# Kernel tuning notes

Measured on AMD Instinct MI355X. Metric: run time of the kernel, lower is better.

## Reference

```python
import jax, jax.numpy as jnp
import numpy as np


def _f_map(x):
    # alpha = ||x||; x normalized; append a constant-1 feature
    alpha = jnp.linalg.norm(x, axis=-1, keepdims=True)
    xn = x / jnp.maximum(alpha, 1e-12)
    ones = jnp.ones(x.shape[:-1] + (1,), x.dtype)
    return jnp.concatenate([(1.0 - 0.5 ** alpha) * xn, ones], axis=-1)


def _mh_lka(q, k, v):
    # kernelized linear attention: cumsum of k (x) v outer products along seq
    q = _f_map(q)  # (B, N, D+1)
    k = _f_map(k)
    kv = jnp.cumsum(jnp.einsum('bnd,bne->bnde', k, v), axis=1)  # (B,N,D+1,D)
    k_ = jnp.cumsum(k, axis=1)
    qk = jnp.einsum('bnd,bnd->bn', q, k_)[..., None]
    qkv = jnp.einsum('bnd,bnde->bne', q, kv)
    return qkv / qk


def _lstm(x, Wih, Whh, bih, bhh):
    # single-layer batch-first LSTM, torch gate order (i, f, g, o)
    B, H = x.shape[0], Whh.shape[1]
    bias = bih + bhh
    def step(carry, xt):
        h, c = carry
        g = xt @ Wih.T + h @ Whh.T + bias  # (B, 4H)
        i, f, gg, o = jnp.split(g, 4, axis=-1)
        c = jax.nn.sigmoid(f) * c + jax.nn.sigmoid(i) * jnp.tanh(gg)
        h = jax.nn.sigmoid(o) * jnp.tanh(c)
        return (h, c), h
    h0 = jnp.zeros((B, H), x.dtype)
    c0 = jnp.zeros((B, H), x.dtype)
    _, hs = jax.lax.scan(step, (h0, c0), x.transpose(1, 0, 2))
    return hs.transpose(1, 0, 2)


def setup_inputs() -> dict:
    in_sz, hid, n_h, out_sz = 512, 64, 8, 512
    B, N = 2, 2048
    key = jax.random.key(0)
    ks = jax.random.split(key, 10)
    s = 0.02
    f32 = jnp.float32
    return {
        'x': jax.random.normal(ks[0], (B, N, in_sz), f32),
        'Wq': jax.random.normal(ks[1], (in_sz, hid * n_h), f32) * s,
        'bq': jnp.zeros((hid * n_h,), f32),
        'Wk': jax.random.normal(ks[2], (in_sz, hid * n_h), f32) * s,
        'bk': jnp.zeros((hid * n_h,), f32),
        'Wv': jax.random.normal(ks[3], (in_sz, hid * n_h), f32) * s,
        'bv': jnp.zeros((hid * n_h,), f32),
        'Wih': jax.random.normal(ks[4], (4 * hid, hid), f32) * s,
        'Whh': jax.random.normal(ks[5], (4 * hid, hid), f32) * s,
        'bih': jnp.zeros((4 * hid,), f32),
        'bhh': jnp.zeros((4 * hid,), f32),
        'W1': jax.random.normal(ks[6], (hid * n_h, out_sz), f32) * s,
        'b1': jnp.zeros((out_sz,), f32),
        'W2': jax.random.normal(ks[7], (out_sz, out_sz), f32) * s,
        'b2': jnp.zeros((out_sz,), f32),
        'gamma': jnp.ones((out_sz,), f32),
        'beta': jnp.zeros((out_sz,), f32),
    }


def reference(x, Wq, bq, Wk, bk, Wv, bv, Wih, Whh, bih, bhh, W1, b1, W2, b2, gamma, beta):
    B, N, _ = x.shape
    H = Whh.shape[1]
    n_h = Wq.shape[1] // H
    def proj(W, b_):
        y = x @ W + b_                              # (B, N, n_h*H)
        return y.reshape(B, N, n_h, H).transpose(0, 2, 1, 3).reshape(B * n_h, N, H)
    q, k, v = proj(Wq, bq), proj(Wk, bk), proj(Wv, bv)
    o = _mh_lka(q, k, v)                            # (B*n_h, N, H)
    o = o + _lstm(o, Wih, Whh, bih, bhh)
    o = o.reshape(B, n_h, N, H).transpose(0, 2, 1, 3).reshape(B, N, n_h * H)
    o = jax.nn.gelu(o @ W1 + b1, approximate=False) @ W2 + b2
    mu = o.mean(-1, keepdims=True)
    var = o.var(-1, keepdims=True)
    return (o - mu) / jnp.sqrt(var + 1e-5) * gamma + beta
```

## Files before the change

### kernel.cpp

```cpp
#include <hip/hip_runtime.h>
#include <hip/hip_bf16.h>
#include <hip/hip_fp16.h>

using bf16 = __hip_bfloat16;
using ushort_t = unsigned short;
using uint32 = unsigned int;
typedef _Float16 f16x2 __attribute__((ext_vector_type(2)));
typedef short short8 __attribute__((ext_vector_type(8)));
typedef float floatx4 __attribute__((ext_vector_type(4)));

__device__ __forceinline__ float u2f(ushort_t u) {
  return __uint_as_float(((unsigned int)u) << 16);
}
__device__ __forceinline__ bool probe_f32(const void* graw) {
  return ((const ushort_t*)graw)[0] != 0x3F80;
}
__device__ __forceinline__ float scrub(float v) {
  return fminf(fmaxf(v, -1e4f), 1e4f);
}
__device__ __forceinline__ short f2b(float x) {
  uint32 u = __float_as_uint(x);
  return (short)((u + 0x7FFFu + ((u >> 16) & 1u)) >> 16);
}
__device__ __forceinline__ float frcp(float x) {
#if __has_builtin(__builtin_amdgcn_rcpf)
  return __builtin_amdgcn_rcpf(x);
#else
  return 1.f / x;
#endif
}
template<int CTRL>
__device__ __forceinline__ float qperm(float x) {
  return __int_as_float(__builtin_amdgcn_mov_dpp(__float_as_int(x), CTRL, 0xF, 0xF, false));
}
__device__ __forceinline__ float fdot2(uint32 a, uint32 b, float c) {
#if __has_builtin(__builtin_amdgcn_fdot2)
  return __builtin_amdgcn_fdot2(__builtin_bit_cast(f16x2, a),
                                __builtin_bit_cast(f16x2, b), c, false);
#else
  const f16x2 av = __builtin_bit_cast(f16x2, a);
  const f16x2 bv = __builtin_bit_cast(f16x2, b);
  return c + (float)av[0] * (float)bv[0] + (float)av[1] * (float)bv[1];
#endif
}

struct Ptrs { const void* p[16]; };
__constant__ const int kCvtTotal = 1347584;

__global__ __launch_bounds__(256) void cvt_k(Ptrs ps, float* __restrict__ dst) {
  const int sizes[16] = {262144,512,262144,512,262144,512,16384,16384,
                         256,256,262144,512,262144,512,512,512};
  int idx = blockIdx.x * 256 + threadIdx.x;
  if (idx >= kCvtTotal) return;
  const bool f32in = probe_f32(ps.p[14]);
  int seg = 0, off = idx;
  while (off >= sizes[seg]) { off -= sizes[seg]; seg++; }
  float v;
  if (f32in) v = ((const float*)ps.p[seg])[off];
  else       v = u2f(((const ushort_t*)ps.p[seg])[off]);
  dst[idx] = v;
}

template<int AMODE, int ACT>
__global__ __launch_bounds__(256) void gemm_mfma(
    const void* __restrict__ A, const float* __restrict__ B,
    const float* __restrict__ bias, const void* __restrict__ graw,
    float* __restrict__ C, int M, int N, int K)
{
  __shared__ __align__(16) short As2[64][36];
  __shared__ __align__(16) short Bs2[64][36];
  const int t = threadIdx.x;
  const int row0 = blockIdx.y * 64, col0 = blockIdx.x * 64;
  const int w = t >> 6, lane = t & 63;
  const int quad = lane >> 4, lr = lane & 15;
  bool f32in = true;
  if (AMODE == 1) f32in = probe_f32(graw);

  const int am = t >> 2, akq = t & 3;
  const int bn = t & 63, bkq = t >> 6;

  floatx4 acc[4] = {{0,0,0,0},{0,0,0,0},{0,0,0,0},{0,0,0,0}};

  for (int k0 = 0; k0 < K; k0 += 32) {
    {
      const size_t aoff = (size_t)(row0 + am) * K + (k0 + akq * 8);
      short8 ap;
      if (AMODE == 0 || f32in) {
        const float4 v0 = *reinterpret_cast<const float4*>((const float*)A + aoff);
        const float4 v1 = *reinterpret_cast<const float4*>((const float*)A + aoff + 4);
        ap[0]=f2b(v0.x); ap[1]=f2b(v0.y); ap[2]=f2b(v0.z); ap[3]=f2b(v0.w);
        ap[4]=f2b(v1.x); ap[5]=f2b(v1.y); ap[6]=f2b(v1.z); ap[7]=f2b(v1.w);
      } else {
        const ushort4 u0 = *reinterpret_cast<const ushort4*>((const ushort_t*)A + aoff);
        const ushort4 u1 = *reinterpret_cast<const ushort4*>((const ushort_t*)A + aoff + 4);
        ap[0]=(short)u0.x; ap[1]=(short)u0.y; ap[2]=(short)u0.z; ap[3]=(short)u0.w;
        ap[4]=(short)u1.x; ap[5]=(short)u1.y; ap[6]=(short)u1.z; ap[7]=(short)u1.w;
      }
      *reinterpret_cast<short8*>(&As2[am][akq * 8]) = ap;
    }
    {
      const float* bp = B + (size_t)(k0 + bkq * 8) * N + col0 + bn;
      short8 bpk;
      #pragma unroll
      for (int j = 0; j < 8; j++) bpk[j] = f2b(bp[(size_t)j * N]);
      *reinterpret_cast<short8*>(&Bs2[bn][bkq * 8]) = bpk;
    }
    __syncthreads();
    {
      const short8 af = *reinterpret_cast<const short8*>(&As2[w * 16 + lr][quad * 8]);
      #pragma unroll
      for (int ct = 0; ct < 4; ct++) {
        const short8 bf = *reinterpret_cast<const short8*>(&Bs2[ct * 16 + lr][quad * 8]);
        acc[ct] = __builtin_amdgcn_mfma_f32_16x16x32_bf16(af, bf, acc[ct], 0, 0, 0);
      }
    }
    __syncthreads();
  }
  #pragma unroll
  for (int ct = 0; ct < 4; ct++) {
    const int col = col0 + ct * 16 + lr;
    const float bb = bias[col];
    #pragma unroll
    for (int r = 0; r < 4; r++) {
      const int row = row0 + w * 16 + quad * 4 + r;
      float v = acc[ct][r] + bb;
      if (ACT == 1) v = 0.5f * v * (1.0f + erff(v * 0.70710678118654752f));
      C[(size_t)row * N + col] = scrub(v);
    }
  }
}

__global__ __launch_bounds__(256) void attn_pass1(
    const float* __restrict__ kb, const float* __restrict__ vb,
    float* __restrict__ S, float* __restrict__ kcS)
{
  const int c = blockIdx.x, bh = blockIdx.y;
  const int b = bh >> 3, hd = bh & 7;
  const int t = threadIdx.x;
  const int e = t & 63, p = t >> 6;

  __shared__ __align__(16) float kf_s[2][64];
  __shared__ __align__(16) float v_s[2][64];

  float Sl[16], kcl[16], S64 = 0.f;
  #pragma unroll
  for (int i = 0; i < 16; i++) { Sl[i] = 0.f; kcl[i] = 0.f; }

  for (int nn = 0; nn < 64; nn++) {
    const int n = c * 64 + nn;
    const int buf = nn & 1;
    if (t < 64) {
      const size_t base = ((size_t)(b * 2048 + n)) * 512 + hd * 64 + t;
      const float kr = kb[base];
      const float vr = vb[base];
      float s = kr * kr;
      #pragma unroll
      for (int off = 32; off > 0; off >>= 1) s += __shfl_xor(s, off);
      const float ak = sqrtf(s);
      kf_s[buf][t] = (1.0f - exp2f(-ak)) / fmaxf(ak, 1e-12f) * kr;
      v_s[buf][t] = vr;
    }
    __syncthreads();
    const float ve = v_s[buf][e];
    #pragma unroll
    for (int i = 0; i < 16; i++) {
      const float kfd = kf_s[buf][p * 16 + i];
      Sl[i]  += kfd * ve;
      kcl[i] += kfd;
    }
    if (p == 0) S64 += ve;
  }
  const size_t sbase = ((size_t)(bh * 32 + c)) * 4160;
  #pragma unroll
  for (int i = 0; i < 16; i++) S[sbase + (p * 16 + i) * 64 + e] = Sl[i];
  if (p == 0) S[sbase + 4096 + e] = S64;
  if (e == 0) {
    const size_t kbase = ((size_t)(bh * 32 + c)) * 64;
    #pragma unroll
    for (int i = 0; i < 16; i++) kcS[kbase + p * 16 + i] = kcl[i];
  }
}

__global__ __launch_bounds__(256) void attn_pass2(
    float* __restrict__ S, float* __restrict__ kcS)
{
  const int bh = blockIdx.y;
  const int idx = blockIdx.x * 256 + threadIdx.x;
  if (idx < 4160) {
    const size_t base = (size_t)bh * 32 * 4160 + idx;
    float v[32];
    #pragma unroll
    for (int cc = 0; cc < 32; cc++) v[cc] = S[base + (size_t)cc * 4160];
    float run = 0.f;
    #pragma unroll
    for (int cc = 0; cc < 32; cc++) { const float tmp = v[cc]; v[cc] = run; run += tmp; }
    #pragma unroll
    for (int cc = 0; cc < 32; cc++) S[base + (size_t)cc * 4160] = v[cc];
  }
  if (blockIdx.x == 0 && threadIdx.x < 64) {
    const size_t base = (size_t)bh * 32 * 64 + threadIdx.x;
    float v[32];
    #pragma unroll
    for (int cc = 0; cc < 32; cc++) v[cc] = kcS[base + (size_t)cc * 64];
    float run = 0.f;
    #pragma unroll
    for (int cc = 0; cc < 32; cc++) { const float tmp = v[cc]; v[cc] = run; run += tmp; }
    #pragma unroll
    for (int cc = 0; cc < 32; cc++) kcS[base + (size_t)cc * 64] = v[cc];
  }
}

__global__ __launch_bounds__(256) void attn_pass3(
    const float* __restrict__ qb, const float* __restrict__ kb, const float* __restrict__ vb,
    const float* __restrict__ S, const float* __restrict__ kcS,
    float* __restrict__ ao)
{
  const int c = blockIdx.x, bh = blockIdx.y;
  const int b = bh >> 3, hd = bh & 7;
  const int t = threadIdx.x;
  const int e = t & 63, p = t >> 6;

  __shared__ __align__(16) float kf_s[2][64], qf_s[2][64], v_s[2][64];
  __shared__ __align__(16) float accp_s[2][4][64];
  __shared__ float qkp_s[2][4];

  float Sl[16], kcl[16], S64;
  {
    const size_t sbase = ((size_t)(bh * 32 + c)) * 4160;
    #pragma unroll
    for (int i = 0; i < 16; i++) Sl[i] = S[sbase + (p * 16 + i) * 64 + e];
    S64 = S[sbase + 4096 + e];
    const size_t kbase = ((size_t)(bh * 32 + c)) * 64;
    #pragma unroll
    for (int i = 0; i < 16; i++) kcl[i] = kcS[kbase + p * 16 + i];
  }

  for (int nn = 0; nn < 64; nn++) {
    const int n = c * 64 + nn;
    const int buf = nn & 1;
    if (t < 64) {
      const size_t base = ((size_t)(b * 2048 + n)) * 512 + hd * 64 + t;
      const float qr = qb[base];
      const float kr = kb[base];
      const float vr = vb[base];
      float sq = qr * qr, sk = kr * kr;
      #pragma unroll
      for (int off = 32; off > 0; off >>= 1) {
        sq += __shfl_xor(sq, off);
        sk += __shfl_xor(sk, off);
      }
      const float aq = sqrtf(sq), ak = sqrtf(sk);
      qf_s[buf][t] = (1.0f - exp2f(-aq)) / fmaxf(aq, 1e-12f) * qr;
      kf_s[buf][t] = (1.0f - exp2f(-ak)) / fmaxf(ak, 1e-12f) * kr;
      v_s[buf][t] = vr;
    }
    __syncthreads();
    const float ve = v_s[buf][e];
    float accp = 0.f, qkp = 0.f;
    #pragma unroll
    for (int i = 0; i < 16; i++) {
      const float kfd = kf_s[buf][p * 16 + i];
      const float qfd = qf_s[buf][p * 16 + i];
      Sl[i]  += kfd * ve;
      accp   += qfd * Sl[i];
      kcl[i] += kfd;
      qkp    += qfd * kcl[i];
    }
    if (p == 0) {
      S64  += ve;
      accp += S64;
      qkp  += (float)(n + 1);
    }
    accp_s[buf][p][e] = accp;
    if (e == 0) qkp_s[buf][p] = qkp;
    __syncthreads();
    if (t < 64) {
      const float num = accp_s[buf][0][t] + accp_s[buf][1][t] +
                        accp_s[buf][2][t] + accp_s[buf][3][t];
      float den = qkp_s[buf][0] + qkp_s[buf][1] + qkp_s[buf][2] + qkp_s[buf][3];
      den = fmaxf(den, 1e-6f);
      ao[((size_t)(bh * 2048 + n)) * 64 + t] = scrub(num / den);
    }
  }
}

__global__ __launch_bounds__(256) void gatesin_k(
    const float* __restrict__ ao, const float* __restrict__ Wihf,
    const float* __restrict__ bihf, const float* __restrict__ bhhf,
    __half* __restrict__ G)
{
  const int t = threadIdx.x;
  const int row0 = blockIdx.x * 16;
  __shared__ __align__(16) float o_s[16 * 64];
  __shared__ __align__(16) __half g_s[16 * 256];
  {
    const float4 v = *reinterpret_cast<const float4*>(ao + (size_t)row0 * 64 + t * 4);
    *reinterpret_cast<float4*>(&o_s[t * 4]) = v;
  }
  float w[64];
  #pragma unroll
  for (int e = 0; e < 64; e++) w[e] = Wihf[t * 64 + e];
  const float bias = bihf[t] + bhhf[t];
  __syncthreads();
  const int p = (t & 63) * 4 + (t >> 6);
  for (int r = 0; r < 16; r++) {
    float acc = bias;
    #pragma unroll
    for (int e4 = 0; e4 < 16; e4++) {
      const float4 o4 = *reinterpret_cast<const float4*>(&o_s[r * 64 + e4 * 4]);
      acc += w[e4*4+0]*o4.x + w[e4*4+1]*o4.y + w[e4*4+2]*o4.z + w[e4*4+3]*o4.w;
    }
    g_s[r * 256 + p] = __float2half(acc);
  }
  __syncthreads();
  const uint4* src = reinterpret_cast<const uint4*>(&g_s[0]);
  uint4* dst = reinterpret_cast<uint4*>(G + (size_t)row0 * 256);
  dst[t] = src[t];
  dst[t + 256] = src[t + 256];
}

__global__ __attribute__((amdgpu_flat_work_group_size(256, 256), amdgpu_waves_per_eu(1, 1)))
void lstm_k(
    const float* __restrict__ ao, const __half* __restrict__ G,
    const float* __restrict__ Whhf, float* __restrict__ y1)
{
  const int bh = blockIdx.x;
  const int b = bh >> 3, hd = bh & 7;
  const int t = threadIdx.x;
  const int gate = t & 3;
  const int e = t >> 2;
  const bool isG = (gate == 2);
  const bool owner = (gate == 0);

  __shared__ __align__(16) _Float16 hh[2][64];
  __shared__ __align__(16) float ao_s[2][16 * 64];

  uint32 w[32];
  {
    const float4* wp = reinterpret_cast<const float4*>(Whhf + (size_t)((gate << 6) + e) * 64);
    #pragma unroll
    for (int i = 0; i < 16; i++) {
      const float4 v = wp[i];
      f16x2 p0; p0[0] = (_Float16)v.x; p0[1] = (_Float16)v.y;
      f16x2 p1; p1[0] = (_Float16)v.z; p1[1] = (_Float16)v.w;
      w[i * 2 + 0] = __builtin_bit_cast(uint32, p0);
      w[i * 2 + 1] = __builtin_bit_cast(uint32, p1);
    }
  }
  #pragma unroll
  for (int i = 0; i < 32; i++) asm volatile("" : "+v"(w[i]));

  float c = 0.f;
  if (t < 64) hh[0][t] = (_Float16)0.f;

  const size_t aobase = (size_t)bh * 2048 * 64;
  const size_t gbase  = (size_t)bh * 2048 * 256;
  const ushort_t* Gu = reinterpret_cast<const ushort_t*>(G);

  float gcur[16];
  {
    const float4 a0 = *reinterpret_cast<const float4*>(ao + aobase + t * 4);
    *reinterpret_cast<float4*>(&ao_s[0][t * 4]) = a0;
    #pragma unroll
    for (int j = 0; j < 16; j++) {
      const ushort_t gu = Gu[gbase + (size_t)j * 256 + t];
      gcur[j] = (float)__builtin_bit_cast(_Float16, gu);
    }
  }
  __syncthreads();

  for (int ch = 0; ch < 128; ch++) {
    const int buf = ch & 1;
    float4 a1; ushort_t gn2[16];
    if (ch + 1 < 128) {
      a1 = *reinterpret_cast<const float4*>(ao + aobase + (size_t)(ch + 1) * 1024 + t * 4);
      #pragma unroll
      for (int j = 0; j < 16; j++)
        gn2[j] = Gu[gbase + (size_t)(ch + 1) * 4096 + (size_t)j * 256 + t];
    }
    #pragma unroll
    for (int nn = 0; nn < 16; nn++) {
      const int n = ch * 16 + nn;
      const int hb = n & 1;
      const float gin = gcur[nn];
      const uint4* hp = reinterpret_cast<const uint4*>(&hh[hb][0]);
      float d0 = 0.f, d1 = 0.f, d2 = 0.f, d3 = 0.f;
      #pragma unroll
      for (int q = 0; q < 8; q++) {
        const uint4 h4 = hp[q];
        d0 = fdot2(w[q * 4 + 0], h4.x, d0);
        d1 = fdot2(w[q * 4 + 1], h4.y, d1);
        d2 = fdot2(w[q * 4 + 2], h4.z, d2);
        d3 = fdot2(w[q * 4 + 3], h4.w, d3);
      }
      const float g = gin + (d0 + d1) + (d2 + d3);
      const float xx = isG ? (2.f * g) : g;
      const float sg = frcp(1.0f + __expf(-xx));
      const float act = isG ? (2.f * sg - 1.f) : sg;
      const float af  = qperm<0xB1>(act);
      const float ag  = qperm<0x4E>(act);
      const float ao4 = qperm<0x1B>(act);
      if (owner) {
        c = af * c + act * ag;
        const float ex = __expf(2.f * c);
        const float tc = 1.f - 2.f * frcp(ex + 1.f);
        const float h = ao4 * tc;
        hh[1 - hb][e] = (_Float16)h;
        y1[((size_t)(b * 2048 + n)) * 512 + hd * 64 + e] =
            scrub(ao_s[buf][nn * 64 + e] + h);
      }
      if (nn == 15 && ch + 1 < 128) {
        const int nb = 1 - buf;
        *reinterpret_cast<float4*>(&ao_s[nb][t * 4]) = a1;
        #pragma unroll
        for (int j = 0; j < 16; j++)
          gcur[j] = (float)__builtin_bit_cast(_Float16, gn2[j]);
      }
      asm volatile("s_waitcnt lgkmcnt(0)\n\ts_barrier" ::: "memory");
    }
  }
}

__global__ __launch_bounds__(256) void ln_k(
    const float* __restrict__ X, const float* __restrict__ gamf,
    const float* __restrict__ betf, const void* __restrict__ graw,
    void* __restrict__ out)
{
  const int r = blockIdx.x;
  const int t = threadIdx.x;
  const bool f32out = probe_f32(graw);
  const float a = X[(size_t)r * 512 + t];
  const float b = X[(size_t)r * 512 + 256 + t];
  float s1 = a + b, s2 = a * a + b * b;
  #pragma unroll
  for (int off = 32; off > 0; off >>= 1) {
    s1 += __shfl_xor(s1, off);
    s2 += __shfl_xor(s2, off);
  }
  __shared__ float sh1[4], sh2[4];
  if ((t & 63) == 0) { sh1[t >> 6] = s1; sh2[t >> 6] = s2; }
  __syncthreads();
  const float tot1 = sh1[0] + sh1[1] + sh1[2] + sh1[3];
  const float tot2 = sh2[0] + sh2[1] + sh2[2] + sh2[3];
  const float mu = tot1 * (1.0f / 512.0f);
  const float var = fmaxf(tot2 * (1.0f / 512.0f) - mu * mu, 0.f);
  const float rs = rsqrtf(var + 1e-5f);
  const float o0 = scrub((a - mu) * rs * gamf[t]       + betf[t]);
  const float o1 = scrub((b - mu) * rs * gamf[256 + t] + betf[256 + t]);
  if (f32out) {
    ((float*)out)[(size_t)r * 512 + t]       = o0;
    ((float*)out)[(size_t)r * 512 + 256 + t] = o1;
  } else {
    ((bf16*)out)[(size_t)r * 512 + t]       = __float2bfloat16(o0);
    ((bf16*)out)[(size_t)r * 512 + 256 + t] = __float2bfloat16(o1);
  }
}

extern "C" void kernel_launch(void* const* d_in, const int* in_sizes, int n_in,
                              void* d_out, int out_size, void* d_ws, size_t ws_size,
                              hipStream_t stream) {
  const void* x    = d_in[0];
  const void* graw = d_in[15];

  float* ws  = (float*)d_ws;
  float* q   = ws;
  float* kb  = q   + 2097152;
  float* v   = kb  + 2097152;
  float* ao  = v   + 2097152;
  float* S   = ao  + 2097152;
  float* kcS = S   + 2129920;
  float* cvt = kcS + 32768;
  float* Wqf  = cvt;            float* bqf  = cvt + 262144;
  float* Wkf  = cvt + 262656;   float* bkf  = cvt + 524800;
  float* Wvf  = cvt + 525312;   float* bvf  = cvt + 787456;
  float* Wihf = cvt + 787968;   float* Whhf = cvt + 804352;
  float* bihf = cvt + 820736;   float* bhhf = cvt + 820992;
  float* W1f  = cvt + 821248;   float* b1f  = cvt + 1083392;
  float* W2f  = cvt + 1083904;  float* b2f_ = cvt + 1346048;
  float* gamf = cvt + 1346560;  float* betf = cvt + 1347072;
  __half* G = (__half*)kb;
  float* y1 = q;
  float* f1 = kb;
  float* f2 = v;

  Ptrs ps;
  for (int i = 0; i < 16; i++) ps.p[i] = d_in[i + 1];

  cvt_k<<<(1347584 + 255) / 256, 256, 0, stream>>>(ps, cvt);

  const dim3 gg(8, 64);
  gemm_mfma<1, 0><<<gg, 256, 0, stream>>>(x, Wqf, bqf, graw, q,  4096, 512, 512);
  gemm_mfma<1, 0><<<gg, 256, 0, stream>>>(x, Wkf, bkf, graw, kb, 4096, 512, 512);
  gemm_mfma<1, 0><<<gg, 256, 0, stream>>>(x, Wvf, bvf, graw, v,  4096, 512, 512);
  attn_pass1<<<dim3(32, 16), 256, 0, stream>>>(kb, v, S, kcS);
  attn_pass2<<<dim3(17, 16), 256, 0, stream>>>(S, kcS);
  attn_pass3<<<dim3(32, 16), 256, 0, stream>>>(q, kb, v, S, kcS, ao);
  gatesin_k<<<2048, 256, 0, stream>>>(ao, Wihf, bihf, bhhf, G);
  lstm_k<<<16, 256, 0, stream>>>(ao, G, Whhf, y1);
  gemm_mfma<0, 1><<<gg, 256, 0, stream>>>(y1, W1f, b1f, graw, f1, 4096, 512, 512);
  gemm_mfma<0, 0><<<gg, 256, 0, stream>>>(f1, W2f, b2f_, graw, f2, 4096, 512, 512);
  ln_k<<<4096, 256, 0, stream>>>(f2, gamf, betf, graw, d_out);
}
```

Baseline: 986.5 us.

## Replace gates-input kernel with MFMA GEMM and bulk-load attention chunks

The LSTM input-gate projection moves from a scalar FMA kernel to the bf16 MFMA GEMM, using a new transposed-B mode and fp16 output. The gate layout changes to natural order, so lstm_k reindexes its G reads. The folded bih+bhh bias is now computed in cvt_k. attn_pass1 and attn_pass3 load and feature-map the whole 64-row chunk into shared memory up front, using all threads, instead of using 64 threads per row with a barrier each step. This adds shared-memory footprint and lowers the precision of the gate GEMM to bf16.

```diff
diff --git a/kernel.cpp b/kernel.cpp
--- a/kernel.cpp
+++ b/kernel.cpp
@@ -45,14 +45,21 @@
 }
 
 struct Ptrs { const void* p[16]; };
-__constant__ const int kCvtTotal = 1347584;
 
 __global__ __launch_bounds__(256) void cvt_k(Ptrs ps, float* __restrict__ dst) {
   const int sizes[16] = {262144,512,262144,512,262144,512,16384,16384,
                          256,256,262144,512,262144,512,512,512};
   int idx = blockIdx.x * 256 + threadIdx.x;
-  if (idx >= kCvtTotal) return;
+  if (idx >= 1347840) return;
   const bool f32in = probe_f32(ps.p[14]);
+  if (idx >= 1347584) {
+    const int i = idx - 1347584;
+    float a, b;
+    if (f32in) { a = ((const float*)ps.p[8])[i]; b = ((const float*)ps.p[9])[i]; }
+    else { a = u2f(((const ushort_t*)ps.p[8])[i]); b = u2f(((const ushort_t*)ps.p[9])[i]); }
+    dst[idx] = a + b;
+    return;
+  }
   int seg = 0, off = idx;
   while (off >= sizes[seg]) { off -= sizes[seg]; seg++; }
   float v;
@@ -61,11 +68,11 @@
   dst[idx] = v;
 }
 
-template<int AMODE, int ACT>
+template<int AMODE, int ACT, int BMODE, int OUT>
 __global__ __launch_bounds__(256) void gemm_mfma(
     const void* __restrict__ A, const float* __restrict__ B,
     const float* __restrict__ bias, const void* __restrict__ graw,
-    float* __restrict__ C, int M, int N, int K)
+    void* __restrict__ Cv, int M, int N, int K)
 {
   __shared__ __align__(16) short As2[64][36];
   __shared__ __align__(16) short Bs2[64][36];
@@ -99,10 +106,18 @@
       *reinterpret_cast<short8*>(&As2[am][akq * 8]) = ap;
     }
     {
-      const float* bp = B + (size_t)(k0 + bkq * 8) * N + col0 + bn;
       short8 bpk;
-      #pragma unroll
-      for (int j = 0; j < 8; j++) bpk[j] = f2b(bp[(size_t)j * N]);
+      if (BMODE == 0) {
+        const float* bp = B + (size_t)(k0 + bkq * 8) * N + col0 + bn;
+        #pragma unroll
+        for (int j = 0; j < 8; j++) bpk[j] = f2b(bp[(size_t)j * N]);
+      } else {
+        const float* bp = B + (size_t)(col0 + bn) * K + k0 + bkq * 8;
+        const float4 v0 = *reinterpret_cast<const float4*>(bp);
+        const float4 v1 = *reinterpret_cast<const float4*>(bp + 4);
+        bpk[0]=f2b(v0.x); bpk[1]=f2b(v0.y); bpk[2]=f2b(v0.z); bpk[3]=f2b(v0.w);
+        bpk[4]=f2b(v1.x); bpk[5]=f2b(v1.y); bpk[6]=f2b(v1.z); bpk[7]=f2b(v1.w);
+      }
       *reinterpret_cast<short8*>(&Bs2[bn][bkq * 8]) = bpk;
     }
     __syncthreads();
@@ -125,7 +140,8 @@
       const int row = row0 + w * 16 + quad * 4 + r;
       float v = acc[ct][r] + bb;
       if (ACT == 1) v = 0.5f * v * (1.0f + erff(v * 0.70710678118654752f));
-      C[(size_t)row * N + col] = scrub(v);
+      if (OUT == 0) ((float*)Cv)[(size_t)row * N + col] = scrub(v);
+      else ((__half*)Cv)[(size_t)row * N + col] = __float2half(scrub(v));
     }
   }
 }
@@ -139,32 +155,31 @@
   const int t = threadIdx.x;
   const int e = t & 63, p = t >> 6;
 
-  __shared__ __align__(16) float kf_s[2][64];
-  __shared__ __align__(16) float v_s[2][64];
+  __shared__ __align__(16) float kf_s[64][64];
+  __shared__ __align__(16) float v_s[64][64];
+
+  for (int r = 0; r < 16; r++) {
+    const int nl = p * 16 + r;
+    const size_t base = ((size_t)(b * 2048 + c * 64 + nl)) * 512 + hd * 64 + e;
+    const float kr = kb[base];
+    const float vr = vb[base];
+    float s = kr * kr;
+    #pragma unroll
+    for (int off = 32; off > 0; off >>= 1) s += __shfl_xor(s, off);
+    const float ak = sqrtf(s);
+    kf_s[nl][e] = (1.0f - exp2f(-ak)) * frcp(fmaxf(ak, 1e-12f)) * kr;
+    v_s[nl][e] = vr;
+  }
+  __syncthreads();
 
   float Sl[16], kcl[16], S64 = 0.f;
   #pragma unroll
   for (int i = 0; i < 16; i++) { Sl[i] = 0.f; kcl[i] = 0.f; }
-
   for (int nn = 0; nn < 64; nn++) {
-    const int n = c * 64 + nn;
-    const int buf = nn & 1;
-    if (t < 64) {
-      const size_t base = ((size_t)(b * 2048 + n)) * 512 + hd * 64 + t;
-      const float kr = kb[base];
-      const float vr = vb[base];
-      float s = kr * kr;
-      #pragma unroll
-      for (int off = 32; off > 0; off >>= 1) s += __shfl_xor(s, off);
-      const float ak = sqrtf(s);
-      kf_s[buf][t] = (1.0f - exp2f(-ak)) / fmaxf(ak, 1e-12f) * kr;
-      v_s[buf][t] = vr;
-    }
-    __syncthreads();
-    const float ve = v_s[buf][e];
+    const float ve = v_s[nn][e];
     #pragma unroll
     for (int i = 0; i < 16; i++) {
-      const float kfd = kf_s[buf][p * 16 + i];
+      const float kfd = kf_s[nn][p * 16 + i];
       Sl[i]  += kfd * ve;
       kcl[i] += kfd;
     }
@@ -220,9 +235,27 @@
   const int t = threadIdx.x;
   const int e = t & 63, p = t >> 6;
 
-  __shared__ __align__(16) float kf_s[2][64], qf_s[2][64], v_s[2][64];
+  __shared__ __align__(16) float qf_s[64][64], kf_s[64][64], v_s[64][64];
   __shared__ __align__(16) float accp_s[2][4][64];
   __shared__ float qkp_s[2][4];
+
+  for (int r = 0; r < 16; r++) {
+    const int nl = p * 16 + r;
+    const size_t base = ((size_t)(b * 2048 + c * 64 + nl)) * 512 + hd * 64 + e;
+    const float qr = qb[base];
+    const float kr = kb[base];
+    const float vr = vb[base];
+    float sq = qr * qr, sk = kr * kr;
+    #pragma unroll
+    for (int off = 32; off > 0; off >>= 1) {
+      sq += __shfl_xor(sq, off);
+      sk += __shfl_xor(sk, off);
+    }
+    const float aq = sqrtf(sq), ak = sqrtf(sk);
+    qf_s[nl][e] = (1.0f - exp2f(-aq)) * frcp(fmaxf(aq, 1e-12f)) * qr;
+    kf_s[nl][e] = (1.0f - exp2f(-ak)) * frcp(fmaxf(ak, 1e-12f)) * kr;
+    v_s[nl][e] = vr;
+  }
 
   float Sl[16], kcl[16], S64;
   {
@@ -234,33 +267,17 @@
     #pragma unroll
     for (int i = 0; i < 16; i++) kcl[i] = kcS[kbase + p * 16 + i];
   }
+  __syncthreads();
 
   for (int nn = 0; nn < 64; nn++) {
     const int n = c * 64 + nn;
     const int buf = nn & 1;
-    if (t < 64) {
-      const size_t base = ((size_t)(b * 2048 + n)) * 512 + hd * 64 + t;
-      const float qr = qb[base];
-      const float kr = kb[base];
-      const float vr = vb[base];
-      float sq = qr * qr, sk = kr * kr;
-      #pragma unroll
-      for (int off = 32; off > 0; off >>= 1) {
-        sq += __shfl_xor(sq, off);
-        sk += __shfl_xor(sk, off);
-      }
-      const float aq = sqrtf(sq), ak = sqrtf(sk);
-      qf_s[buf][t] = (1.0f - exp2f(-aq)) / fmaxf(aq, 1e-12f) * qr;
-      kf_s[buf][t] = (1.0f - exp2f(-ak)) / fmaxf(ak, 1e-12f) * kr;
-      v_s[buf][t] = vr;
-    }
-    __syncthreads();
-    const float ve = v_s[buf][e];
+    const float ve = v_s[nn][e];
     float accp = 0.f, qkp = 0.f;
     #pragma unroll
     for (int i = 0; i < 16; i++) {
-      const float kfd = kf_s[buf][p * 16 + i];
-      const float qfd = qf_s[buf][p * 16 + i];
+      const float kfd = kf_s[nn][p * 16 + i];
+      const float qfd = qf_s[nn][p * 16 + i];
       Sl[i]  += kfd * ve;
       accp   += qfd * Sl[i];
       kcl[i] += kfd;
@@ -284,41 +301,6 @@
   }
 }
 
-__global__ __launch_bounds__(256) void gatesin_k(
-    const float* __restrict__ ao, const float* __restrict__ Wihf,
-    const float* __restrict__ bihf, const float* __restrict__ bhhf,
-    __half* __restrict__ G)
-{
-  const int t = threadIdx.x;
-  const int row0 = blockIdx.x * 16;
-  __shared__ __align__(16) float o_s[16 * 64];
-  __shared__ __align__(16) __half g_s[16 * 256];
-  {
-    const float4 v = *reinterpret_cast<const float4*>(ao + (size_t)row0 * 64 + t * 4);
-    *reinterpret_cast<float4*>(&o_s[t * 4]) = v;
-  }
-  float w[64];
-  #pragma unroll
-  for (int e = 0; e < 64; e++) w[e] = Wihf[t * 64 + e];
-  const float bias = bihf[t] + bhhf[t];
-  __syncthreads();
-  const int p = (t & 63) * 4 + (t >> 6);
-  for (int r = 0; r < 16; r++) {
-    float acc = bias;
-    #pragma unroll
-    for (int e4 = 0; e4 < 16; e4++) {
-      const float4 o4 = *reinterpret_cast<const float4*>(&o_s[r * 64 + e4 * 4]);
-      acc += w[e4*4+0]*o4.x + w[e4*4+1]*o4.y + w[e4*4+2]*o4.z + w[e4*4+3]*o4.w;
-    }
-    g_s[r * 256 + p] = __float2half(acc);
-  }
-  __syncthreads();
-  const uint4* src = reinterpret_cast<const uint4*>(&g_s[0]);
-  uint4* dst = reinterpret_cast<uint4*>(G + (size_t)row0 * 256);
-  dst[t] = src[t];
-  dst[t + 256] = src[t + 256];
-}
-
 __global__ __attribute__((amdgpu_flat_work_group_size(256, 256), amdgpu_waves_per_eu(1, 1)))
 void lstm_k(
     const float* __restrict__ ao, const __half* __restrict__ G,
@@ -329,6 +311,7 @@
   const int t = threadIdx.x;
   const int gate = t & 3;
   const int e = t >> 2;
+  const int jg = gate * 64 + e;
   const bool isG = (gate == 2);
   const bool owner = (gate == 0);
 
@@ -337,7 +320,7 @@
 
   uint32 w[32];
   {
-    const float4* wp = reinterpret_cast<const float4*>(Whhf + (size_t)((gate << 6) + e) * 64);
+    const float4* wp = reinterpret_cast<const float4*>(Whhf + (size_t)jg * 64);
     #pragma unroll
     for (int i = 0; i < 16; i++) {
       const float4 v = wp[i];
@@ -363,7 +346,7 @@
     *reinterpret_cast<float4*>(&ao_s[0][t * 4]) = a0;
     #pragma unroll
     for (int j = 0; j < 16; j++) {
-      const ushort_t gu = Gu[gbase + (size_t)j * 256 + t];
+      const ushort_t gu = Gu[gbase + (size_t)j * 256 + jg];
       gcur[j] = (float)__builtin_bit_cast(_Float16, gu);
     }
   }
@@ -376,7 +359,7 @@
       a1 = *reinterpret_cast<const float4*>(ao + aobase + (size_t)(ch + 1) * 1024 + t * 4);
       #pragma unroll
       for (int j = 0; j < 16; j++)
-        gn2[j] = Gu[gbase + (size_t)(ch + 1) * 4096 + (size_t)j * 256 + t];
+        gn2[j] = Gu[gbase + (size_t)(ch + 1) * 4096 + (size_t)j * 256 + jg];
     }
     #pragma unroll
     for (int nn = 0; nn < 16; nn++) {
@@ -474,10 +457,10 @@
   float* Wkf  = cvt + 262656;   float* bkf  = cvt + 524800;
   float* Wvf  = cvt + 525312;   float* bvf  = cvt + 787456;
   float* Wihf = cvt + 787968;   float* Whhf = cvt + 804352;
-  float* bihf = cvt + 820736;   float* bhhf = cvt + 820992;
   float* W1f  = cvt + 821248;   float* b1f  = cvt + 1083392;
   float* W2f  = cvt + 1083904;  float* b2f_ = cvt + 1346048;
   float* gamf = cvt + 1346560;  float* betf = cvt + 1347072;
+  float* bsum = cvt + 1347584;
   __half* G = (__half*)kb;
   float* y1 = q;
   float* f1 = kb;
@@ -486,18 +469,18 @@
   Ptrs ps;
   for (int i = 0; i < 16; i++) ps.p[i] = d_in[i + 1];
 
-  cvt_k<<<(1347584 + 255) / 256, 256, 0, stream>>>(ps, cvt);
+  cvt_k<<<(1347840 + 255) / 256, 256, 0, stream>>>(ps, cvt);
 
   const dim3 gg(8, 64);
-  gemm_mfma<1, 0><<<gg, 256, 0, stream>>>(x, Wqf, bqf, graw, q,  4096, 512, 512);
-  gemm_mfma<1, 0><<<gg, 256, 0, stream>>>(x, Wkf, bkf, graw, kb, 4096, 512, 512);
-  gemm_mfma<1, 0><<<gg, 256, 0, stream>>>(x, Wvf, bvf, graw, v,  4096, 512, 512);
+  gemm_mfma<1, 0, 0, 0><<<gg, 256, 0, stream>>>(x, Wqf, bqf, graw, q,  4096, 512, 512);
+  gemm_mfma<1, 0, 0, 0><<<gg, 256, 0, stream>>>(x, Wkf, bkf, graw, kb, 4096, 512, 512);
+  gemm_mfma<1, 0, 0, 0><<<gg, 256, 0, stream>>>(x, Wvf, bvf, graw, v,  4096, 512, 512);
   attn_pass1<<<dim3(32, 16), 256, 0, stream>>>(kb, v, S, kcS);
   attn_pass2<<<dim3(17, 16), 256, 0, stream>>>(S, kcS);
   attn_pass3<<<dim3(32, 16), 256, 0, stream>>>(q, kb, v, S, kcS, ao);
-  gatesin_k<<<2048, 256, 0, stream>>>(ao, Wihf, bihf, bhhf, G);
+  gemm_mfma<0, 0, 1, 1><<<dim3(4, 512), 256, 0, stream>>>(ao, Wihf, bsum, graw, G, 32768, 256, 64);
   lstm_k<<<16, 256, 0, stream>>>(ao, G, Whhf, y1);
-  gemm_mfma<0, 1><<<gg, 256, 0, stream>>>(y1, W1f, b1f, graw, f1, 4096, 512, 512);
-  gemm_mfma<0, 0><<<gg, 256, 0, stream>>>(f1, W2f, b2f_, graw, f2, 4096, 512, 512);
+  gemm_mfma<0, 1, 0, 0><<<gg, 256, 0, stream>>>(y1, W1f, b1f, graw, f1, 4096, 512, 512);
+  gemm_mfma<0, 0, 0, 0><<<gg, 256, 0, stream>>>(f1, W2f, b2f_, graw, f2, 4096, 512, 512);
   ln_k<<<4096, 256, 0, stream>>>(f2, gamf, betf, graw, d_out);
 }
```

After: 923.4 us. 6.4% less time.
